# Optimization experiments

Measured on AMD Instinct MI355X. Metric: run time of the kernel, lower is better.

Reference implementation:

```python
import jax, jax.numpy as jnp
import numpy as np

B, DIM, HEADS, HH, WW = 4, 256, 8, 48, 48
N = HH * WW
CS = DIM // 4  # channels per crpe split / lowpass split = 64
POOL_SIZES = (1, 2, 3, 6)


def _constrain(kern, k):
    # kern: (C, C, k*k-1); insert the constrained -1 center tap, reshape to OIHW
    C = kern.shape[0]
    ctr = (k * k) // 2
    full = jnp.concatenate(
        [kern[:, :, :ctr], -jnp.ones((C, C, 1), kern.dtype), kern[:, :, ctr:]], axis=2)
    return full.reshape(C, C, k, k)


def _conv(x, w, k):
    p = k // 2
    return jax.lax.conv_general_dilated(
        x, w, (1, 1), [(p, p), (p, p)],
        dimension_numbers=('NCHW', 'OIHW', 'NCHW'))


def _upsample_bilinear_ac(x, H, W):
    # bilinear, align_corners=True, from (B,C,sh,sw) to (B,C,H,W)
    Bc, Cc, sh, sw = x.shape
    if sh == 1 and sw == 1:
        return jnp.broadcast_to(x, (Bc, Cc, H, W))
    ys = jnp.arange(H, dtype=x.dtype) * ((sh - 1) / (H - 1))
    xs = jnp.arange(W, dtype=x.dtype) * ((sw - 1) / (W - 1))
    y0 = jnp.floor(ys).astype(jnp.int32)
    x0 = jnp.floor(xs).astype(jnp.int32)
    y1 = jnp.minimum(y0 + 1, sh - 1)
    x1 = jnp.minimum(x0 + 1, sw - 1)
    wy = (ys - y0.astype(x.dtype))[:, None]
    wx = (xs - x0.astype(x.dtype))[None, :]
    v00 = x[:, :, y0[:, None], x0[None, :]]
    v01 = x[:, :, y0[:, None], x1[None, :]]
    v10 = x[:, :, y1[:, None], x0[None, :]]
    v11 = x[:, :, y1[:, None], x1[None, :]]
    return (v00 * (1 - wy) * (1 - wx) + v01 * (1 - wy) * wx
            + v10 * wy * (1 - wx) + v11 * wy * wx)


def _lowpass(v):
    # v: (B,C,H,W); H,W divisible by all pool sizes -> adaptive pool == uniform block mean
    Bc, Cc, Hc, Wc = v.shape
    outs = []
    for c, s in zip(jnp.split(v, 4, axis=1), POOL_SIZES):
        p = c.reshape(Bc, Cc // 4, s, Hc // s, s, Wc // s).mean(axis=(3, 5))
        outs.append(_upsample_bilinear_ac(p, Hc, Wc))
    return jax.nn.relu(jnp.concatenate(outs, axis=1))


def _crpe(q, res, Hc, Wc, kern3, kern5, kern7):
    # q: (B,h,N,Ch); res: (B,N,C)
    Bc, h, Nc, Ch = q.shape
    C = h * Ch
    v = res.transpose(0, 2, 1).reshape(Bc, C, Hc, Wc)
    lp = _lowpass(v)
    v0, v1, v2, v3 = jnp.split(v, 4, axis=1)
    conv_v = jnp.concatenate([
        v0,
        _conv(v1, _constrain(kern3, 3), 3),
        _conv(v2, _constrain(kern5, 5), 5),
        _conv(v3, _constrain(kern7, 7), 7)], axis=1)
    conv_v = conv_v.reshape(Bc, h, Ch, Nc).transpose(0, 1, 3, 2)  # B h N Ch
    lp = lp.reshape(Bc, h, Ch, Nc).transpose(0, 1, 3, 2)
    return q * conv_v + lp


def setup_inputs() -> dict:
    key = jax.random.key(0)
    ks = jax.random.split(key, 9)
    x = jax.random.normal(ks[0], (B, N, DIM), jnp.float32)
    wq = jax.random.normal(ks[1], (DIM, DIM), jnp.float32) * 0.02
    wkv = jax.random.normal(ks[2], (2 * DIM, DIM), jnp.float32) * 0.02
    wres = jax.random.normal(ks[3], (DIM, DIM), jnp.float32) * 0.02
    wproj = jax.random.normal(ks[4], (DIM, DIM), jnp.float32) * 0.02
    bproj = jnp.zeros((DIM,), jnp.float32)
    def base_kernel(k, kk):
        kern = jax.random.uniform(k, (CS, CS, kk * kk - 1), jnp.float32)
        return kern / kern.sum(axis=2, keepdims=True)
    kern3 = base_kernel(ks[5], 3)
    kern5 = base_kernel(ks[6], 5)
    kern7 = base_kernel(ks[7], 7)
    return {'x': x, 'H': HH, 'W': WW, 'wq': wq, 'wkv': wkv, 'wres': wres,
            'wproj': wproj, 'bproj': bproj, 'kern3': kern3, 'kern5': kern5,
            'kern7': kern7}


def reference(x, H, W, wq, wkv, wres, wproj, bproj, kern3, kern5, kern7):
    Bc, Nc, C = x.shape
    h = HEADS
    Ch = C // h
    scale = Ch ** -0.5
    q = (x @ wq.T).reshape(Bc, Nc, h, Ch).transpose(0, 2, 1, 3)          # B h N Ch
    kv = (x @ wkv.T).reshape(Bc, Nc, 2, h, Ch).transpose(2, 0, 3, 1, 4)  # 2 B h N Ch
    k, v = kv[0], kv[1]
    attn = jax.nn.softmax(jnp.einsum('bhnc,bhmc->bhnm', q * scale, k), axis=-1)
    res = jax.nn.relu(x @ wres.T)
    crpe = _crpe(q, res, H, W, kern3, kern5, kern7)
    out = (jnp.einsum('bhnm,bhmc->bhnc', attn, v) + crpe)
    out = out.transpose(0, 2, 1, 3).reshape(Bc, Nc, C)
    return out @ wproj.T + bproj
```

## Files before the change

### kernel.cpp

```cpp
#include <hip/hip_runtime.h>
#include <math.h>

#define NTOK 2304
#define DIMC 256

typedef __attribute__((ext_vector_type(8))) short short8;
typedef __attribute__((ext_vector_type(4))) float f32x4;

__device__ __forceinline__ unsigned short f2bf(float f) {
  unsigned u = __float_as_uint(f);
  u += 0x7fffu + ((u >> 16) & 1u);
  return (unsigned short)(u >> 16);
}
__device__ __forceinline__ float bf2f(unsigned short h) {
  return __uint_as_float(((unsigned)h) << 16);
}
__device__ __forceinline__ unsigned pack2(float a, float b) {
  return (unsigned)f2bf(a) | ((unsigned)f2bf(b) << 16);
}
__device__ __forceinline__ float fexp2(float x) {
#if __has_builtin(__builtin_amdgcn_exp2f)
  return __builtin_amdgcn_exp2f(x);
#else
  return exp2f(x);
#endif
}
__device__ __forceinline__ void split4(float4 v, uint2& hp, uint2& lp) {
  unsigned short h0 = f2bf(v.x), h1 = f2bf(v.y), h2 = f2bf(v.z), h3 = f2bf(v.w);
  unsigned short l0 = f2bf(v.x - bf2f(h0)), l1 = f2bf(v.y - bf2f(h1));
  unsigned short l2 = f2bf(v.z - bf2f(h2)), l3 = f2bf(v.w - bf2f(h3));
  hp.x = (unsigned)h0 | ((unsigned)h1 << 16);
  hp.y = (unsigned)h2 | ((unsigned)h3 << 16);
  lp.x = (unsigned)l0 | ((unsigned)l1 << 16);
  lp.y = (unsigned)l2 | ((unsigned)l3 << 16);
}

__global__ __launch_bounds__(256) void k_prep_all(
    const float* __restrict__ x, const float* __restrict__ wq,
    const float* __restrict__ wkv, const float* __restrict__ wres,
    const float* __restrict__ wproj, const float* __restrict__ k3,
    const float* __restrict__ k5, const float* __restrict__ k7,
    unsigned short* __restrict__ xhi, unsigned short* __restrict__ xlo,
    unsigned short* __restrict__ Whi, unsigned short* __restrict__ Wlo,
    unsigned short* __restrict__ pwhi, unsigned short* __restrict__ pwlo,
    unsigned short* __restrict__ wT) {
  int bx = blockIdx.x;
  int tid = threadIdx.x;
  if (bx < 2304) {
    int i = bx * 256 + tid;
    uint2 hp, lp;
    split4(((const float4*)x)[i], hp, lp);
    ((uint2*)xhi)[i] = hp;
    ((uint2*)xlo)[i] = lp;
  } else if (bx < 2560) {
    int idx = (bx - 2304) * 256 + tid;
    int row = idx >> 6, q4 = idx & 63;
    const float* src;
    if (row < 256)      src = wq + (size_t)row * 256;
    else if (row < 768) src = wkv + (size_t)(row - 256) * 256;
    else                src = wres + (size_t)(row - 768) * 256;
    uint2 hp, lp;
    split4(*(const float4*)(src + q4 * 4), hp, lp);
    ((uint2*)Whi)[idx] = hp;
    ((uint2*)Wlo)[idx] = lp;
  } else if (bx < 2624) {
    int idx = (bx - 2560) * 256 + tid;
    uint2 hp, lp;
    split4(((const float4*)wproj)[idx], hp, lp);
    ((uint2*)pwhi)[idx] = hp;
    ((uint2*)pwlo)[idx] = lp;
  } else {
    int idx = (bx - 2624) * 256 + tid;
    const float* src; int K, tloc;
    if (idx < 9 * 4096)       { K = 3; src = k3; tloc = idx >> 12; }
    else if (idx < 34 * 4096) { K = 5; src = k5; tloc = (idx - 9 * 4096) >> 12; }
    else                      { K = 7; src = k7; tloc = (idx - 34 * 4096) >> 12; }
    int r = idx & 4095, oc = r >> 6, ic = r & 63;
    int K2 = K * K, ctr = K2 / 2;
    float v = (tloc == ctr) ? -1.f
            : src[((size_t)oc * 64 + ic) * (K2 - 1) + (tloc < ctr ? tloc : tloc - 1)];
    wT[idx] = f2bf(v);
  }
}

__global__ __launch_bounds__(512, 2) void k_gemm_qkvres_mfma(
    const unsigned short* __restrict__ xhi, const unsigned short* __restrict__ xlo,
    const unsigned short* __restrict__ Whi, const unsigned short* __restrict__ Wlo,
    float* __restrict__ qb, unsigned short* __restrict__ khi,
    unsigned short* __restrict__ klo, unsigned short* __restrict__ vT,
    float* __restrict__ resb, unsigned short* __restrict__ resT) {
  __shared__ __align__(16) unsigned short Ah[128 * 64];
  __shared__ __align__(16) unsigned short Al[128 * 64];
  __shared__ __align__(16) unsigned short Bh[128 * 64];
  __shared__ __align__(16) unsigned short Bl[128 * 64];
  const int tid = threadIdx.x;
  const int row0 = blockIdx.x * 128;
  const int col0 = blockIdx.y * 128;
  const int w = tid >> 6, lane = tid & 63, lg = lane >> 4, lc = lane & 15;
  const int wm = w >> 1, wn = w & 1;

  f32x4 acc[2][4];
#pragma unroll
  for (int i = 0; i < 2; ++i)
#pragma unroll
    for (int j = 0; j < 4; ++j) acc[i][j] = (f32x4){0.f, 0.f, 0.f, 0.f};

  for (int kc = 0; kc < 256; kc += 64) {
    __syncthreads();
#pragma unroll
    for (int l = 0; l < 2; ++l) {
      int idx = tid + l * 512;
      int r = idx >> 3, o = idx & 7;
      int sl = ((o ^ (r & 7))) * 8;
      *(uint4*)&Ah[r * 64 + sl] = *(const uint4*)&xhi[(size_t)(row0 + r) * 256 + kc + o * 8];
      *(uint4*)&Al[r * 64 + sl] = *(const uint4*)&xlo[(size_t)(row0 + r) * 256 + kc + o * 8];
      *(uint4*)&Bh[r * 64 + sl] = *(const uint4*)&Whi[(size_t)(col0 + r) * 256 + kc + o * 8];
      *(uint4*)&Bl[r * 64 + sl] = *(const uint4*)&Wlo[(size_t)(col0 + r) * 256 + kc + o * 8];
    }
    __syncthreads();
#pragma unroll
    for (int ks = 0; ks < 2; ++ks) {
      short8 ah[2], al[2], bh[4], bl[4];
#pragma unroll
      for (int mi = 0; mi < 2; ++mi) {
        int r = wm * 32 + mi * 16 + lc;
        int sl = (((ks * 4 + lg) ^ (r & 7))) * 8;
        ah[mi] = *(short8*)&Ah[r * 64 + sl];
        al[mi] = *(short8*)&Al[r * 64 + sl];
      }
#pragma unroll
      for (int ni = 0; ni < 4; ++ni) {
        int r = wn * 64 + ni * 16 + lc;
        int sl = (((ks * 4 + lg) ^ (r & 7))) * 8;
        bh[ni] = *(short8*)&Bh[r * 64 + sl];
        bl[ni] = *(short8*)&Bl[r * 64 + sl];
      }
#pragma unroll
      for (int mi = 0; mi < 2; ++mi)
#pragma unroll
        for (int ni = 0; ni < 4; ++ni) {
          acc[mi][ni] = __builtin_amdgcn_mfma_f32_16x16x32_bf16(ah[mi], bh[ni], acc[mi][ni], 0, 0, 0);
          acc[mi][ni] = __builtin_amdgcn_mfma_f32_16x16x32_bf16(ah[mi], bl[ni], acc[mi][ni], 0, 0, 0);
          acc[mi][ni] = __builtin_amdgcn_mfma_f32_16x16x32_bf16(al[mi], bh[ni], acc[mi][ni], 0, 0, 0);
        }
    }
  }

#pragma unroll
  for (int mi = 0; mi < 2; ++mi) {
    int rbase = row0 + wm * 32 + mi * 16 + lg * 4;
#pragma unroll
    for (int ni = 0; ni < 4; ++ni) {
      int col = col0 + wn * 64 + ni * 16 + lc;
#pragma unroll
      for (int j = 0; j < 4; ++j) {
        int row = rbase + j;
        int b = row / NTOK, n = row % NTOK;
        float vv = acc[mi][ni][j];
        if (col < 256) {
          int head = col >> 5, ch = col & 31;
          qb[(((size_t)b * 8 + head) * NTOK + n) * 32 + ch] = vv;
        } else if (col < 512) {
          int o = col - 256; int head = o >> 5, ch = o & 31;
          size_t idx = (((size_t)b * 8 + head) * NTOK + n) * 32 + ch;
          unsigned short h = f2bf(vv);
          khi[idx] = h;
          klo[idx] = f2bf(vv - bf2f(h));
        } else if (col < 768) {
          int o = col - 512; int head = o >> 5, ch = o & 31;
          vT[(((size_t)b * 8 + head) * 32 + ch) * NTOK + n] = f2bf(vv);
        } else {
          int c = col - 768;
          float rv = fmaxf(vv, 0.f);
          resb[((size_t)b * 256 + c) * NTOK + n] = rv;
          if (c >= 64) {
            int g = (c >> 6) - 1, ic = c & 63;
            resT[(((size_t)b * 3 + g) * NTOK + n) * 64 + ic] = f2bf(rv);
          }
        }
      }
    }
  }
}

__device__ __forceinline__ void softmax_pv(
    f32x4 (&s)[8], float& m_r, float& l_r, f32x4& o0, f32x4& o1,
    int lg, int lc, int srcA, unsigned short (*vs)[136]) {
  float mx[8];
#pragma unroll
  for (int nt = 0; nt < 8; ++nt)
    mx[nt] = fmaxf(fmaxf(s[nt][0], s[nt][1]), fmaxf(s[nt][2], s[nt][3]));
  float mloc = fmaxf(fmaxf(fmaxf(mx[0], mx[1]), fmaxf(mx[2], mx[3])),
                     fmaxf(fmaxf(mx[4], mx[5]), fmaxf(mx[6], mx[7])));

  if (__any(mloc > m_r + 8.f)) {
    float mt = mloc;
    mt = fmaxf(mt, __shfl_xor(mt, 16, 64));
    mt = fmaxf(mt, __shfl_xor(mt, 32, 64));
    float mn = fmaxf(m_r, mt);
    float corr = fexp2(m_r - mn);
    m_r = mn;
    l_r *= corr;
#pragma unroll
    for (int j = 0; j < 4; ++j) {
      float cj = __shfl(corr, lg * 4 + j, 64);
      o0[j] *= cj;
      o1[j] *= cj;
    }
  }

  float ls = 0.f;
#pragma unroll
  for (int nt = 0; nt < 8; ++nt)
#pragma unroll
    for (int j = 0; j < 4; ++j) {
      float p = fexp2(s[nt][j] - m_r);
      s[nt][j] = p;
      ls += p;
    }
  l_r += ls;

  unsigned W[8][2];
#pragma unroll
  for (int nt = 0; nt < 8; ++nt) {
    W[nt][0] = pack2(s[nt][0], s[nt][1]);
    W[nt][1] = pack2(s[nt][2], s[nt][3]);
  }

  __builtin_amdgcn_s_setprio(1);
#pragma unroll
  for (int h2 = 0; h2 < 4; ++h2) {
    unsigned v0 = (lg & 2) ? W[2 * h2 + 1][0] : W[2 * h2][0];
    unsigned v1 = (lg & 2) ? W[2 * h2 + 1][1] : W[2 * h2][1];
    union { unsigned u[4]; short8 v; } pa;
    pa.u[0] = (unsigned)__shfl((int)v0, srcA, 64);
    pa.u[1] = (unsigned)__shfl((int)v1, srcA, 64);
    pa.u[2] = (unsigned)__shfl((int)v0, srcA + 16, 64);
    pa.u[3] = (unsigned)__shfl((int)v1, srcA + 16, 64);
    short8 vf0 = *(short8*)&vs[lc][h2 * 32 + lg * 8];
    short8 vf1 = *(short8*)&vs[lc + 16][h2 * 32 + lg * 8];
    o0 = __builtin_amdgcn_mfma_f32_16x16x32_bf16(pa.v, vf0, o0, 0, 0, 0);
    o1 = __builtin_amdgcn_mfma_f32_16x16x32_bf16(pa.v, vf1, o1, 0, 0, 0);
  }
  __builtin_amdgcn_s_setprio(0);
}

__device__ __forceinline__ void attn_body(
    int bh, int qt, int tid,
    const float* __restrict__ qb, const unsigned short* __restrict__ khi,
    const unsigned short* __restrict__ klo, const unsigned short* __restrict__ vT,
    float* __restrict__ accb,
    unsigned short (*ks_hi)[40], unsigned short (*vs)[136]) {
  const int r0 = qt * 64;
  const int w = tid >> 6;
  const int lane = tid & 63;
  const int lg = lane >> 4;
  const int lc = lane & 15;

  const float scale = 0.17677669529663688f * 1.4426950408889634f;

  const float* qp = qb + (((size_t)bh * NTOK + r0 + w * 16 + lc) * 32 + lg * 8);
  float qf[8];
  *(float4*)&qf[0] = *(const float4*)qp;
  *(float4*)&qf[4] = *(const float4*)(qp + 4);
  short8 qh, ql;
#pragma unroll
  for (int i = 0; i < 8; ++i) {
    float v = qf[i] * scale;
    unsigned short h = f2bf(v);
    qh[i] = (short)h;
    ql[i] = (short)f2bf(v - bf2f(h));
  }

  float m_r = -1.0e30f;
  float l_r = 0.f;
  f32x4 o0 = {0.f, 0.f, 0.f, 0.f};
  f32x4 o1 = {0.f, 0.f, 0.f, 0.f};

  const int krow = tid >> 1, kseg = (tid & 1) * 16;
  const int vrow = tid >> 3, vseg = (tid & 7) * 16;

  const unsigned short* khs = khi + ((size_t)bh * NTOK + krow) * 32 + kseg;
  const unsigned short* vsrc = vT + ((size_t)bh * 32 + vrow) * NTOK + vseg;
  const unsigned short* klp = klo + ((size_t)bh * NTOK + lc) * 32 + lg * 8;

  uint4 ph0 = *(const uint4*)khs,  ph1 = *(const uint4*)(khs + 8);
  uint4 pv0 = *(const uint4*)vsrc, pv1 = *(const uint4*)(vsrc + 8);

  const int srcA = ((lg & 1) * 2) * 16 + lc;

  for (int kt = 0; kt < 18; ++kt) {
    const int kv0 = kt * 128;
    __syncthreads();
    *(uint4*)&ks_hi[krow][kseg]     = ph0;
    *(uint4*)&ks_hi[krow][kseg + 8] = ph1;
    *(uint4*)&vs[vrow][vseg]        = pv0;
    *(uint4*)&vs[vrow][vseg + 8]    = pv1;
    __syncthreads();

    if (kt < 17) {
      size_t ko = (size_t)(kt + 1) * 128 * 32;
      int vo = (kt + 1) * 128;
      ph0 = *(const uint4*)(khs + ko);  ph1 = *(const uint4*)(khs + ko + 8);
      pv0 = *(const uint4*)(vsrc + vo); pv1 = *(const uint4*)(vsrc + vo + 8);
    }

    f32x4 s[8];
#pragma unroll
    for (int half = 0; half < 2; ++half) {
      short8 klr[4];
#pragma unroll
      for (int q = 0; q < 4; ++q)
        klr[q] = *(const short8*)(klp + (size_t)(kv0 + (half * 4 + q) * 16) * 32);
      __builtin_amdgcn_s_setprio(1);
#pragma unroll
      for (int q = 0; q < 4; ++q) {
        int nt = half * 4 + q;
        short8 kh = *(short8*)&ks_hi[nt * 16 + lc][lg * 8];
        f32x4 a = {0.f, 0.f, 0.f, 0.f};
        a = __builtin_amdgcn_mfma_f32_16x16x32_bf16(kh, qh, a, 0, 0, 0);
        a = __builtin_amdgcn_mfma_f32_16x16x32_bf16(klr[q], qh, a, 0, 0, 0);
        a = __builtin_amdgcn_mfma_f32_16x16x32_bf16(kh, ql, a, 0, 0, 0);
        s[nt] = a;
      }
      __builtin_amdgcn_s_setprio(0);
    }

    softmax_pv(s, m_r, l_r, o0, o1, lg, lc, srcA, vs);
  }

  float lfull = l_r;
  lfull += __shfl_xor(lfull, 16, 64);
  lfull += __shfl_xor(lfull, 32, 64);

  float* op = accb + ((size_t)bh * NTOK + r0 + w * 16) * 32;
#pragma unroll
  for (int j = 0; j < 4; ++j) {
    float lj = __shfl(lfull, lg * 4 + j, 64);
    float inv = 1.f / lj;
    int r = lg * 4 + j;
    op[r * 32 + lc] = o0[j] * inv;
    op[r * 32 + lc + 16] = o1[j] * inv;
  }
}

template <int K>
__device__ __forceinline__ void conv_body(
    const unsigned short* __restrict__ plane,
    const unsigned short* __restrict__ wTg,
    float* __restrict__ outg,
    int y, int w, int lane, unsigned short* lds) {
  constexpr int P = K / 2;
  const int tid = w * 64 + lane;
  const int lg = lane >> 4, lc = lane & 15;
  const int oc0 = w * 16;

  uint4 zz = {0, 0, 0, 0};
  for (int i = tid; i < K * 224; i += 256) ((uint4*)lds)[i] = zz;
  __syncthreads();

  f32x4 acc[3];
  acc[0] = acc[1] = acc[2] = (f32x4){0.f, 0.f, 0.f, 0.f};

#pragma unroll
  for (int c = 0; c < 2; ++c) {
    for (int idx = tid; idx < K * 192; idx += 256) {
      int i = idx / 192, rem = idx % 192;
      int gx = rem >> 2, o = rem & 3;
      int gy = y + i - P;
      if ((unsigned)gy < 48u) {
        uint4 v = *(const uint4*)(plane + ((size_t)(gy * 48 + gx)) * 64 + c * 32 + o * 8);
        int slot = gx + P;
        *(uint4*)(lds + ((size_t)i * 56 + slot) * 32 + ((o ^ ((slot >> 1) & 3)) * 8)) = v;
      }
    }
    __syncthreads();

    for (int ky = 0; ky < K; ++ky) {
#pragma unroll
      for (int kx = 0; kx < K; ++kx) {
        const int tap = ky * K + kx;
        short8 aw = *(const short8*)(wTg + (size_t)tap * 4096 + (oc0 + lc) * 64 +
                                     c * 32 + lg * 8);
#pragma unroll
        for (int u = 0; u < 3; ++u) {
          int slot = u * 16 + lc + kx;
          short8 bv = *(short8*)(lds + ((size_t)(ky * 56 + slot)) * 32 +
                                 ((lg ^ ((slot >> 1) & 3)) * 8));
          acc[u] = __builtin_amdgcn_mfma_f32_16x16x32_bf16(aw, bv, acc[u], 0, 0, 0);
        }
      }
    }
    __syncthreads();
  }

#pragma unroll
  for (int u = 0; u < 3; ++u)
#pragma unroll
    for (int j = 0; j < 4; ++j)
      outg[(size_t)(oc0 + lg * 4 + j) * NTOK + y * 48 + u * 16 + lc] = acc[u][j];
}

__device__ __forceinline__ void pool_body(
    const float* __restrict__ resb, float* __restrict__ pooled,
    int task, int lane) {
  const int sArr[4] = {1, 2, 3, 6};
  int g = task >> 8, rem = task & 255;
  int b = rem >> 6, cc = rem & 63;
  int c = g * 64 + cc;
  int S = sArr[g];
  int WSZ = 48 / S, NPX = WSZ * WSZ;
  const float* src = resb + ((size_t)b * 256 + c) * NTOK;
  const float inv = 1.f / NPX;
  for (int w = 0; w < S * S; ++w) {
    int wy = w / S, wx = w % S;
    float sum = 0.f;
    for (int idx = lane; idx < NPX; idx += 64) {
      int yy = wy * WSZ + idx / WSZ;
      int xx = wx * WSZ + idx % WSZ;
      sum += src[yy * 48 + xx];
    }
#pragma unroll
    for (int msk = 1; msk < 64; msk <<= 1) sum += __shfl_xor(sum, msk, 64);
    if (lane == 0) pooled[((size_t)b * 256 + c) * 36 + w] = sum * inv;
  }
}

__global__ __launch_bounds__(256, 4) void k_fat(
    const float* __restrict__ qb, const unsigned short* __restrict__ khi,
    const unsigned short* __restrict__ klo, const unsigned short* __restrict__ vT,
    float* __restrict__ accb, const unsigned short* __restrict__ resT,
    const unsigned short* __restrict__ wT, float* __restrict__ convb,
    const float* __restrict__ resb, float* __restrict__ pooled) {
  __shared__ __align__(16) unsigned char smem[25088];
  const int bx = blockIdx.x;
  const int tid = threadIdx.x;
  if (bx < 1152) {
    unsigned short (*ks_hi)[40] = (unsigned short(*)[40])(smem);
    unsigned short (*vs)[136]   = (unsigned short(*)[136])(smem + 10240);
    attn_body(bx & 31, bx >> 5, tid, qb, khi, klo, vT, accb, ks_hi, vs);
  } else if (bx < 1728) {
    int cid = bx - 1152;
    int g = cid % 3, rest = cid / 3;
    int b = rest / 48, y = rest % 48;
    const unsigned short* plane = resT + (((size_t)b * 3 + g) * NTOK) * 64;
    float* outg = convb + ((size_t)b * 192 + g * 64) * NTOK;
    unsigned short* lds = (unsigned short*)smem;
    int w = tid >> 6, lane = tid & 63;
    if (g == 0)      conv_body<3>(plane, wT,             outg, y, w, lane, lds);
    else if (g == 1) conv_body<5>(plane, wT + 9 * 4096,  outg, y, w, lane, lds);
    else             conv_body<7>(plane, wT + 34 * 4096, outg, y, w, lane, lds);
  } else {
    int task = (bx - 1728) * 4 + (tid >> 6);
    pool_body(resb, pooled, task, tid & 63);
  }
}

__global__ void k_combine(
    const float* __restrict__ qb, const float* __restrict__ accb,
    const float* __restrict__ resb, const float* __restrict__ convb,
    const float* __restrict__ pooled, unsigned short* __restrict__ preh,
    unsigned short* __restrict__ prel) {
  int nt = blockIdx.x;
  int head = blockIdx.y;
  int b = blockIdx.z;
  int tid = threadIdx.x;
  int n = nt * 8 + (tid >> 5);
  int ch = tid & 31;
  int c = head * 32 + ch;
  int g = c >> 6;
  const int sArr[4] = {1, 2, 3, 6};
  int s = sArr[g];

  size_t qidx = (((size_t)b * 8 + head) * NTOK + n) * 32 + ch;
  float qv = qb[qidx];
  float av = accb[qidx];
  float cvv = (g == 0) ? resb[((size_t)b * 256 + c) * NTOK + n]
                       : convb[((size_t)b * 192 + (c - 64)) * NTOK + n];
  const float* pl = pooled + ((size_t)b * 256 + c) * 36;
  float lp;
  if (s == 1) {
    lp = pl[0];
  } else {
    int yy = n / 48, xx = n % 48;
    float fs = (float)(s - 1) / 47.0f;
    float ry = yy * fs, rx = xx * fs;
    int y0 = (int)ry, x0 = (int)rx;
    int y1 = min(y0 + 1, s - 1), x1 = min(x0 + 1, s - 1);
    float wy = ry - (float)y0, wx = rx - (float)x0;
    float v00 = pl[y0 * s + x0], v01 = pl[y0 * s + x1];
    float v10 = pl[y1 * s + x0], v11 = pl[y1 * s + x1];
    lp = v00 * (1 - wy) * (1 - wx) + v01 * (1 - wy) * wx +
         v10 * wy * (1 - wx) + v11 * wy * wx;
  }
  lp = fmaxf(lp, 0.f);
  float val = av + qv * cvv + lp;
  unsigned short h = f2bf(val);
  size_t oidx = ((size_t)b * NTOK + n) * 256 + c;
  preh[oidx] = h;
  prel[oidx] = f2bf(val - bf2f(h));
}

__global__ __launch_bounds__(512, 2) void k_gemm_proj_mfma(
    const unsigned short* __restrict__ preh, const unsigned short* __restrict__ prel,
    const unsigned short* __restrict__ pwhi, const unsigned short* __restrict__ pwlo,
    const float* __restrict__ bproj, float* __restrict__ outp) {
  __shared__ __align__(16) unsigned short Ah[128 * 64];
  __shared__ __align__(16) unsigned short Al[128 * 64];
  __shared__ __align__(16) unsigned short Bh[128 * 64];
  __shared__ __align__(16) unsigned short Bl[128 * 64];
  const int tid = threadIdx.x;
  const int row0 = blockIdx.x * 128;
  const int col0 = blockIdx.y * 128;
  const int w = tid >> 6, lane = tid & 63, lg = lane >> 4, lc = lane & 15;
  const int wm = w >> 1, wn = w & 1;

  f32x4 acc[2][4];
#pragma unroll
  for (int i = 0; i < 2; ++i)
#pragma unroll
    for (int j = 0; j < 4; ++j) acc[i][j] = (f32x4){0.f, 0.f, 0.f, 0.f};

  for (int kc = 0; kc < 256; kc += 64) {
    __syncthreads();
#pragma unroll
    for (int l = 0; l < 2; ++l) {
      int idx = tid + l * 512;
      int r = idx >> 3, o = idx & 7;
      int sl = ((o ^ (r & 7))) * 8;
      *(uint4*)&Ah[r * 64 + sl] = *(const uint4*)&preh[(size_t)(row0 + r) * 256 + kc + o * 8];
      *(uint4*)&Al[r * 64 + sl] = *(const uint4*)&prel[(size_t)(row0 + r) * 256 + kc + o * 8];
      *(uint4*)&Bh[r * 64 + sl] = *(const uint4*)&pwhi[(size_t)(col0 + r) * 256 + kc + o * 8];
      *(uint4*)&Bl[r * 64 + sl] = *(const uint4*)&pwlo[(size_t)(col0 + r) * 256 + kc + o * 8];
    }
    __syncthreads();
#pragma unroll
    for (int ks = 0; ks < 2; ++ks) {
      short8 ah[2], al[2], bh[4], bl[4];
#pragma unroll
      for (int mi = 0; mi < 2; ++mi) {
        int r = wm * 32 + mi * 16 + lc;
        int sl = (((ks * 4 + lg) ^ (r & 7))) * 8;
        ah[mi] = *(short8*)&Ah[r * 64 + sl];
        al[mi] = *(short8*)&Al[r * 64 + sl];
      }
#pragma unroll
      for (int ni = 0; ni < 4; ++ni) {
        int r = wn * 64 + ni * 16 + lc;
        int sl = (((ks * 4 + lg) ^ (r & 7))) * 8;
        bh[ni] = *(short8*)&Bh[r * 64 + sl];
        bl[ni] = *(short8*)&Bl[r * 64 + sl];
      }
#pragma unroll
      for (int mi = 0; mi < 2; ++mi)
#pragma unroll
        for (int ni = 0; ni < 4; ++ni) {
          acc[mi][ni] = __builtin_amdgcn_mfma_f32_16x16x32_bf16(ah[mi], bh[ni], acc[mi][ni], 0, 0, 0);
          acc[mi][ni] = __builtin_amdgcn_mfma_f32_16x16x32_bf16(ah[mi], bl[ni], acc[mi][ni], 0, 0, 0);
          acc[mi][ni] = __builtin_amdgcn_mfma_f32_16x16x32_bf16(al[mi], bh[ni], acc[mi][ni], 0, 0, 0);
        }
    }
  }

#pragma unroll
  for (int mi = 0; mi < 2; ++mi) {
    int rbase = row0 + wm * 32 + mi * 16 + lg * 4;
#pragma unroll
    for (int ni = 0; ni < 4; ++ni) {
      int col = col0 + wn * 64 + ni * 16 + lc;
#pragma unroll
      for (int j = 0; j < 4; ++j)
        outp[(size_t)(rbase + j) * 256 + col] = acc[mi][ni][j] + bproj[col];
    }
  }
}

extern "C" void kernel_launch(void* const* d_in, const int* in_sizes, int n_in,
                              void* d_out, int out_size, void* d_ws, size_t ws_size,
                              hipStream_t stream) {
  const float* x     = (const float*)d_in[0];
  const float* wq    = (const float*)d_in[3];
  const float* wkv   = (const float*)d_in[4];
  const float* wres  = (const float*)d_in[5];
  const float* wproj = (const float*)d_in[6];
  const float* bproj = (const float*)d_in[7];
  const float* kern3 = (const float*)d_in[8];
  const float* kern5 = (const float*)d_in[9];
  const float* kern7 = (const float*)d_in[10];

  const size_t SZ = (size_t)4 * 8 * NTOK * 32;
  float* wsf  = (float*)d_ws;
  float* qb   = wsf;
  float* resb = wsf + SZ;
  float* accb = wsf + 2 * SZ;
  unsigned short* xhi = (unsigned short*)(wsf + 2 * SZ);
  unsigned short* xlo = (unsigned short*)(wsf + 2 * SZ + SZ / 2);
  unsigned short* khi = (unsigned short*)(wsf + 3 * SZ);
  unsigned short* klo = (unsigned short*)(wsf + 3 * SZ + SZ / 2);
  unsigned short* vT  = (unsigned short*)(wsf + 4 * SZ);
  unsigned short* resT = (unsigned short*)(wsf + 4 * SZ + SZ / 2);
  unsigned short* wT   = (unsigned short*)(wsf + 4 * SZ + SZ / 2 + 884736);
  unsigned short* Whi = (unsigned short*)(wsf + 4 * SZ + SZ / 2 + 884736 + 169984);
  unsigned short* Wlo = Whi + 262144;
  unsigned short* preh = (unsigned short*)(wsf + 4 * SZ + SZ / 2);
  unsigned short* prel = (unsigned short*)(wsf + 5 * SZ);
  float* convb  = wsf + SZ * 11 / 2;
  float* pooled = convb + 1769472;
  unsigned short* pwhi = (unsigned short*)(pooled + 36864);
  unsigned short* pwlo = pwhi + 65536;
  float* outp = (float*)d_out;

  k_prep_all<<<dim3(3952), 256, 0, stream>>>(x, wq, wkv, wres, wproj, kern3,
                                             kern5, kern7, xhi, xlo, Whi, Wlo,
                                             pwhi, pwlo, wT);
  k_gemm_qkvres_mfma<<<dim3(72, 8), 512, 0, stream>>>(xhi, xlo, Whi, Wlo, qb, khi,
                                                      klo, vT, resb, resT);
  k_fat<<<dim3(1984), 256, 0, stream>>>(qb, khi, klo, vT, accb, resT, wT, convb,
                                        resb, pooled);
  k_combine<<<dim3(288, 8, 4), 256, 0, stream>>>(qb, accb, resb, convb, pooled,
                                                 preh, prel);
  k_gemm_proj_mfma<<<dim3(72, 2), 512, 0, stream>>>(preh, prel, pwhi, pwlo, bproj, outp);
}
```

Baseline: 171.0 us.

## Use hardware bf16 pack, tile conv by column segments, halve proj GEMM rows

```diff
diff --git a/kernel.cpp b/kernel.cpp
--- a/kernel.cpp
+++ b/kernel.cpp
@@ -15,8 +15,10 @@
 __device__ __forceinline__ float bf2f(unsigned short h) {
   return __uint_as_float(((unsigned)h) << 16);
 }
-__device__ __forceinline__ unsigned pack2(float a, float b) {
-  return (unsigned)f2bf(a) | ((unsigned)f2bf(b) << 16);
+__device__ __forceinline__ unsigned cvt_pk_bf16(float lo, float hi) {
+  unsigned r;
+  asm("v_cvt_pk_bf16_f32 %0, %1, %2" : "=v"(r) : "v"(lo), "v"(hi));
+  return r;
 }
 __device__ __forceinline__ float fexp2(float x) {
 #if __has_builtin(__builtin_amdgcn_exp2f)
@@ -223,8 +225,8 @@
   unsigned W[8][2];
 #pragma unroll
   for (int nt = 0; nt < 8; ++nt) {
-    W[nt][0] = pack2(s[nt][0], s[nt][1]);
-    W[nt][1] = pack2(s[nt][2], s[nt][3]);
+    W[nt][0] = cvt_pk_bf16(s[nt][0], s[nt][1]);
+    W[nt][1] = cvt_pk_bf16(s[nt][2], s[nt][3]);
   }
 
   __builtin_amdgcn_s_setprio(1);
@@ -351,54 +353,42 @@
     float* __restrict__ outg,
     int y, int w, int lane, unsigned short* lds) {
   constexpr int P = K / 2;
+  constexpr int SLOTS = 16 + 2 * P;
   const int tid = w * 64 + lane;
   const int lg = lane >> 4, lc = lane & 15;
   const int oc0 = w * 16;
 
-  uint4 zz = {0, 0, 0, 0};
-  for (int i = tid; i < K * 224; i += 256) ((uint4*)lds)[i] = zz;
-  __syncthreads();
-
-  f32x4 acc[3];
-  acc[0] = acc[1] = acc[2] = (f32x4){0.f, 0.f, 0.f, 0.f};
-
-#pragma unroll
-  for (int c = 0; c < 2; ++c) {
-    for (int idx = tid; idx < K * 192; idx += 256) {
-      int i = idx / 192, rem = idx % 192;
-      int gx = rem >> 2, o = rem & 3;
-      int gy = y + i - P;
-      if ((unsigned)gy < 48u) {
-        uint4 v = *(const uint4*)(plane + ((size_t)(gy * 48 + gx)) * 64 + c * 32 + o * 8);
-        int slot = gx + P;
-        *(uint4*)(lds + ((size_t)i * 56 + slot) * 32 + ((o ^ ((slot >> 1) & 3)) * 8)) = v;
-      }
-    }
-    __syncthreads();
-
-    for (int ky = 0; ky < K; ++ky) {
-#pragma unroll
-      for (int kx = 0; kx < K; ++kx) {
-        const int tap = ky * K + kx;
-        short8 aw = *(const short8*)(wTg + (size_t)tap * 4096 + (oc0 + lc) * 64 +
-                                     c * 32 + lg * 8);
-#pragma unroll
-        for (int u = 0; u < 3; ++u) {
-          int slot = u * 16 + lc + kx;
-          short8 bv = *(short8*)(lds + ((size_t)(ky * 56 + slot)) * 32 +
+  for (int t = 0; t < 3; ++t) {
+    f32x4 acc = {0.f, 0.f, 0.f, 0.f};
+#pragma unroll
+    for (int c = 0; c < 2; ++c) {
+      __syncthreads();
+      for (int idx = tid; idx < K * SLOTS * 4; idx += 256) {
+        int i = idx / (SLOTS * 4), rem = idx % (SLOTS * 4);
+        int slot = rem >> 2, o = rem & 3;
+        int gy = y + i - P, gx = t * 16 + slot - P;
+        uint4 v = {0, 0, 0, 0};
+        if ((unsigned)gy < 48u && (unsigned)gx < 48u)
+          v = *(const uint4*)(plane + ((size_t)(gy * 48 + gx)) * 64 + c * 32 + o * 8);
+        *(uint4*)(lds + ((size_t)(i * SLOTS + slot)) * 32 + ((o ^ ((slot >> 1) & 3)) * 8)) = v;
+      }
+      __syncthreads();
+      for (int ky = 0; ky < K; ++ky) {
+#pragma unroll
+        for (int kx = 0; kx < K; ++kx) {
+          short8 aw = *(const short8*)(wTg + (size_t)(ky * K + kx) * 4096 +
+                                       (oc0 + lc) * 64 + c * 32 + lg * 8);
+          int slot = lc + kx;
+          short8 bv = *(short8*)(lds + ((size_t)(ky * SLOTS + slot)) * 32 +
                                  ((lg ^ ((slot >> 1) & 3)) * 8));
-          acc[u] = __builtin_amdgcn_mfma_f32_16x16x32_bf16(aw, bv, acc[u], 0, 0, 0);
+          acc = __builtin_amdgcn_mfma_f32_16x16x32_bf16(aw, bv, acc, 0, 0, 0);
         }
       }
     }
-    __syncthreads();
-  }
-
-#pragma unroll
-  for (int u = 0; u < 3; ++u)
 #pragma unroll
     for (int j = 0; j < 4; ++j)
-      outg[(size_t)(oc0 + lg * 4 + j) * NTOK + y * 48 + u * 16 + lc] = acc[u][j];
+      outg[(size_t)(oc0 + lg * 4 + j) * NTOK + y * 48 + t * 16 + lc] = acc[j];
+  }
 }
 
 __device__ __forceinline__ void pool_body(
@@ -432,7 +422,7 @@
     float* __restrict__ accb, const unsigned short* __restrict__ resT,
     const unsigned short* __restrict__ wT, float* __restrict__ convb,
     const float* __restrict__ resb, float* __restrict__ pooled) {
-  __shared__ __align__(16) unsigned char smem[25088];
+  __shared__ __align__(16) unsigned char smem[18944];
   const int bx = blockIdx.x;
   const int tid = threadIdx.x;
   if (bx < 1152) {
@@ -505,38 +495,42 @@
     const unsigned short* __restrict__ preh, const unsigned short* __restrict__ prel,
     const unsigned short* __restrict__ pwhi, const unsigned short* __restrict__ pwlo,
     const float* __restrict__ bproj, float* __restrict__ outp) {
-  __shared__ __align__(16) unsigned short Ah[128 * 64];
-  __shared__ __align__(16) unsigned short Al[128 * 64];
+  __shared__ __align__(16) unsigned short Ah[64 * 64];
+  __shared__ __align__(16) unsigned short Al[64 * 64];
   __shared__ __align__(16) unsigned short Bh[128 * 64];
   __shared__ __align__(16) unsigned short Bl[128 * 64];
   const int tid = threadIdx.x;
-  const int row0 = blockIdx.x * 128;
+  const int row0 = blockIdx.x * 64;
   const int col0 = blockIdx.y * 128;
   const int w = tid >> 6, lane = tid & 63, lg = lane >> 4, lc = lane & 15;
-  const int wm = w >> 1, wn = w & 1;
-
-  f32x4 acc[2][4];
+  const int wm = w >> 2, wn = w & 3;
+
+  f32x4 acc[2][2];
 #pragma unroll
   for (int i = 0; i < 2; ++i)
 #pragma unroll
-    for (int j = 0; j < 4; ++j) acc[i][j] = (f32x4){0.f, 0.f, 0.f, 0.f};
+    for (int j = 0; j < 2; ++j) acc[i][j] = (f32x4){0.f, 0.f, 0.f, 0.f};
 
   for (int kc = 0; kc < 256; kc += 64) {
     __syncthreads();
+    {
+      int r = tid >> 3, o = tid & 7;
+      int sl = ((o ^ (r & 7))) * 8;
+      *(uint4*)&Ah[r * 64 + sl] = *(const uint4*)&preh[(size_t)(row0 + r) * 256 + kc + o * 8];
+      *(uint4*)&Al[r * 64 + sl] = *(const uint4*)&prel[(size_t)(row0 + r) * 256 + kc + o * 8];
+    }
 #pragma unroll
     for (int l = 0; l < 2; ++l) {
       int idx = tid + l * 512;
       int r = idx >> 3, o = idx & 7;
       int sl = ((o ^ (r & 7))) * 8;
-      *(uint4*)&Ah[r * 64 + sl] = *(const uint4*)&preh[(size_t)(row0 + r) * 256 + kc + o * 8];
-      *(uint4*)&Al[r * 64 + sl] = *(const uint4*)&prel[(size_t)(row0 + r) * 256 + kc + o * 8];
       *(uint4*)&Bh[r * 64 + sl] = *(const uint4*)&pwhi[(size_t)(col0 + r) * 256 + kc + o * 8];
       *(uint4*)&Bl[r * 64 + sl] = *(const uint4*)&pwlo[(size_t)(col0 + r) * 256 + kc + o * 8];
     }
     __syncthreads();
 #pragma unroll
     for (int ks = 0; ks < 2; ++ks) {
-      short8 ah[2], al[2], bh[4], bl[4];
+      short8 ah[2], al[2], bh[2], bl[2];
 #pragma unroll
       for (int mi = 0; mi < 2; ++mi) {
         int r = wm * 32 + mi * 16 + lc;
@@ -545,8 +539,8 @@
         al[mi] = *(short8*)&Al[r * 64 + sl];
       }
 #pragma unroll
-      for (int ni = 0; ni < 4; ++ni) {
-        int r = wn * 64 + ni * 16 + lc;
+      for (int ni = 0; ni < 2; ++ni) {
+        int r = wn * 32 + ni * 16 + lc;
         int sl = (((ks * 4 + lg) ^ (r & 7))) * 8;
         bh[ni] = *(short8*)&Bh[r * 64 + sl];
         bl[ni] = *(short8*)&Bl[r * 64 + sl];
@@ -554,7 +548,7 @@
 #pragma unroll
       for (int mi = 0; mi < 2; ++mi)
 #pragma unroll
-        for (int ni = 0; ni < 4; ++ni) {
+        for (int ni = 0; ni < 2; ++ni) {
           acc[mi][ni] = __builtin_amdgcn_mfma_f32_16x16x32_bf16(ah[mi], bh[ni], acc[mi][ni], 0, 0, 0);
           acc[mi][ni] = __builtin_amdgcn_mfma_f32_16x16x32_bf16(ah[mi], bl[ni], acc[mi][ni], 0, 0, 0);
           acc[mi][ni] = __builtin_amdgcn_mfma_f32_16x16x32_bf16(al[mi], bh[ni], acc[mi][ni], 0, 0, 0);
@@ -566,8 +560,8 @@
   for (int mi = 0; mi < 2; ++mi) {
     int rbase = row0 + wm * 32 + mi * 16 + lg * 4;
 #pragma unroll
-    for (int ni = 0; ni < 4; ++ni) {
-      int col = col0 + wn * 64 + ni * 16 + lc;
+    for (int ni = 0; ni < 2; ++ni) {
+      int col = col0 + wn * 32 + ni * 16 + lc;
 #pragma unroll
       for (int j = 0; j < 4; ++j)
         outp[(size_t)(rbase + j) * 256 + col] = acc[mi][ni][j] + bproj[col];
@@ -619,5 +613,5 @@
                                         resb, pooled);
   k_combine<<<dim3(288, 8, 4), 256, 0, stream>>>(qb, accb, resb, convb, pooled,
                                                  preh, prel);
-  k_gemm_proj_mfma<<<dim3(72, 2), 512, 0, stream>>>(preh, prel, pwhi, pwlo, bproj, outp);
-}
+  k_gemm_proj_mfma<<<dim3(144, 2), 512, 0, stream>>>(preh, prel, pwhi, pwlo, bproj, outp);
+}
```

Measured after the change: 260.0 us. 1.52x slower.
